# Kernel optimization log

Hardware: AMD Instinct MI355X
Metric: run time of the kernel (lower is better)

## Reference

```python
import jax, jax.numpy as jnp
import numpy as np

D_MODEL = 1024
N_HEADS = 16
HEAD_DIM = D_MODEL // N_HEADS


def setup_inputs() -> dict:
    key = jax.random.key(0)
    ks = jax.random.split(key, 5)
    B, S = 4, 2048
    scale = 1.0 / np.sqrt(D_MODEL)
    return {
        "x": jax.random.normal(ks[0], (B, S, D_MODEL), dtype=jnp.float32),
        "wq": jax.random.normal(ks[1], (D_MODEL, D_MODEL), dtype=jnp.float32) * scale,
        "wk": jax.random.normal(ks[2], (D_MODEL, D_MODEL), dtype=jnp.float32) * scale,
        "wv": jax.random.normal(ks[3], (D_MODEL, D_MODEL), dtype=jnp.float32) * scale,
        "wo": jax.random.normal(ks[4], (D_MODEL, D_MODEL), dtype=jnp.float32) * scale,
    }


def reference(x, wq, wk, wv, wo):
    B, S, _ = x.shape
    # projections: x @ W.T, then split heads -> [B, H, S, hd]
    def split_heads(t):
        return t.reshape(B, S, N_HEADS, HEAD_DIM).transpose(0, 2, 1, 3)

    q = split_heads(x @ wq.T)
    k = split_heads(x @ wk.T)
    v = split_heads(x @ wv.T)

    # scores [B, H, S, S], causal mask, stable softmax
    score = jnp.einsum("bhqd,bhkd->bhqk", q, k) / np.sqrt(HEAD_DIM)
    causal = jnp.tril(jnp.ones((S, S), dtype=bool))
    score = jnp.where(causal, score, -jnp.inf)
    attn = jax.nn.softmax(score, axis=-1)

    out = jnp.einsum("bhqk,bhkd->bhqd", attn, v)
    out = out.transpose(0, 2, 1, 3).reshape(B, S, D_MODEL)
    return out @ wo.T
```

## Files before the change

### kernel.cpp

```cpp
#include <hip/hip_runtime.h>
#include <type_traits>


typedef unsigned short u16;
typedef __attribute__((ext_vector_type(8))) short s8;
typedef __attribute__((ext_vector_type(4))) float f4;

#if __has_builtin(__builtin_amdgcn_exp2f)
#define EXP2(x) __builtin_amdgcn_exp2f(x)
#else
#define EXP2(x) exp2f(x)
#endif

__device__ __forceinline__ u16 f2bf(float f) {
    union { float f; unsigned u; } v; v.f = f;
    unsigned r = v.u + 0x7fffu + ((v.u >> 16) & 1u);
    return (u16)(r >> 16);
}

__device__ __forceinline__ unsigned pack_bf2(float a, float b) {
    return __builtin_amdgcn_perm(__float_as_uint(b), __float_as_uint(a),
                                 0x07060302u);
}

__device__ __forceinline__ void cp16(const void* g, void* l) {
    __builtin_amdgcn_global_load_lds(
        (const __attribute__((address_space(1))) unsigned int*)g,
        (__attribute__((address_space(3))) unsigned int*)l, 16, 0, 0);
}

__device__ __forceinline__ s8 load8f(const float* p) {
    const float4 lo = *(const float4*)p;
    const float4 hi = *(const float4*)(p + 4);
    s8 r;
    r[0] = (short)f2bf(lo.x); r[1] = (short)f2bf(lo.y);
    r[2] = (short)f2bf(lo.z); r[3] = (short)f2bf(lo.w);
    r[4] = (short)f2bf(hi.x); r[5] = (short)f2bf(hi.y);
    r[6] = (short)f2bf(hi.z); r[7] = (short)f2bf(hi.w);
    return r;
}

__global__ __launch_bounds__(256)
void f32_to_bf16(const float* __restrict__ in, u16* __restrict__ out, int n8)
{
    const int i = blockIdx.x * 256 + threadIdx.x;
    if (i < n8) *(s8*)(out + (size_t)i * 8) = load8f(in + (size_t)i * 8);
}

__global__ __launch_bounds__(256)
void cvt_w3(const float* __restrict__ a, const float* __restrict__ b2,
            const float* __restrict__ c3, u16* __restrict__ o, int per)
{
    const int y = blockIdx.y;
    const float* src = (y == 0) ? a : ((y == 1) ? b2 : c3);
    u16* dst = o + (size_t)y * per;
    const int i = blockIdx.x * 256 + threadIdx.x;
    *(s8*)(dst + (size_t)i * 8) = load8f(src + (size_t)i * 8);
}

template<typename TC>
__global__ __launch_bounds__(256)
void gemm_bb(const u16* __restrict__ A,
             const u16* __restrict__ W0, const u16* __restrict__ W1,
             const u16* __restrict__ W2,
             TC* __restrict__ C0, TC* __restrict__ C1,
             u16* __restrict__ VT, int K, float cscale)
{
    __shared__ u16 As[3][128 * 32];
    __shared__ u16 Bs[3][128 * 32];

    const int t  = threadIdx.x;
    const int bm = blockIdx.x;
    const int nglob = blockIdx.y * 128;

    const u16* W; int nloc, mode;
    if (nglob < 1024)      { W = W0; nloc = nglob;        mode = 0; }
    else if (nglob < 2048) { W = W1; nloc = nglob - 1024; mode = 1; }
    else                   { W = W2; nloc = nglob - 2048; mode = 2; }

    const int lane = t & 63, w = t >> 6;
    const int wm = (w >> 1) * 64, wn = (w & 1) * 64;
    const int quad = lane >> 4, l16 = lane & 15;

    const int sc = (((lane & 3) ^ ((lane >> 3) & 3))) * 8;
    const int sr = w * 32 + (lane >> 2);
    const u16* Ag0 = A + (size_t)(bm * 128 + sr) * K + sc;
    const u16* Ag1 = Ag0 + (size_t)16 * K;
    const u16* Wg0 = W + (size_t)(nloc + sr) * K + sc;
    const u16* Wg1 = Wg0 + (size_t)16 * K;
    const int la0 = (w * 32) * 32;
    const int la1 = (w * 32 + 16) * 32;

    const int ca = (quad ^ ((l16 >> 1) & 3)) * 8;

    auto stage = [&](int buf, int k0) {
        cp16(Ag0 + k0, &As[buf][la0]);
        cp16(Ag1 + k0, &As[buf][la1]);
        cp16(Wg0 + k0, &Bs[buf][la0]);
        cp16(Wg1 + k0, &Bs[buf][la1]);
    };

    f4 acc[4][4];
    for (int i = 0; i < 4; i++)
        for (int j = 0; j < 4; j++)
            acc[i][j] = (f4){0.f, 0.f, 0.f, 0.f};

    stage(0, 0);
    stage(1, 32);
    int cur = 0;
    for (int k0 = 0; k0 < K; k0 += 32) {
        if (k0 + 32 < K) asm volatile("s_waitcnt vmcnt(4)" ::: "memory");
        else             asm volatile("s_waitcnt vmcnt(0)" ::: "memory");
        __builtin_amdgcn_s_barrier();
        if (k0 + 96 <= K) stage((cur + 2) % 3, k0 + 64);

        s8 af[4], bf[4];
        for (int i = 0; i < 4; i++)
            af[i] = *(const s8*)&As[cur][(wm + i * 16 + l16) * 32 + ca];
        for (int j = 0; j < 4; j++)
            bf[j] = *(const s8*)&Bs[cur][(wn + j * 16 + l16) * 32 + ca];
        for (int i = 0; i < 4; i++)
            for (int j = 0; j < 4; j++)
                acc[i][j] = __builtin_amdgcn_mfma_f32_16x16x32_bf16(
                                af[i], bf[j], acc[i][j], 0, 0, 0);
        cur = (cur == 2) ? 0 : cur + 1;
    }

    if (mode == 2) {
        for (int i = 0; i < 4; i++) {
            const int row0 = bm * 128 + wm + i * 16 + quad * 4;
            const int b = row0 >> 11, s = row0 & 2047;
            for (int j = 0; j < 4; j++) {
                const int n = nloc + wn + j * 16 + l16;
                const int h = n >> 6, d = n & 63;
                unsigned lo = ((unsigned)f2bf(acc[i][j][1]) << 16) | f2bf(acc[i][j][0]);
                unsigned hi = ((unsigned)f2bf(acc[i][j][3]) << 16) | f2bf(acc[i][j][2]);
                *(uint2*)(VT + ((size_t)((b * 16 + h) * 64 + d)) * 2048 + s) =
                    make_uint2(lo, hi);
            }
        }
    } else {
        TC* C = (mode == 0) ? C0 : C1;
        const float cs = (mode == 0) ? cscale : 1.0f;
        for (int i = 0; i < 4; i++) {
            const int row = bm * 128 + wm + i * 16 + quad * 4;
            for (int j = 0; j < 4; j++) {
                const int col = nloc + wn + j * 16 + l16;
                for (int r = 0; r < 4; r++) {
                    const float val = acc[i][j][r] * cs;
                    if constexpr (std::is_same<TC, float>::value)
                        C[(size_t)(row + r) * 1024 + col] = val;
                    else
                        C[(size_t)(row + r) * 1024 + col] = f2bf(val);
                }
            }
        }
    }
}

#define PSTR 72

__global__ __launch_bounds__(256)
void attn_q32(const u16* __restrict__ Q, const u16* __restrict__ K,
              const u16* __restrict__ Vt, u16* __restrict__ O)
{
    __shared__ u16 Ks[2][64 * 64];
    __shared__ u16 Vs[2][64 * 64];
    __shared__ u16 Ps[4][32 * PSTR];

    const int bh = blockIdx.x;
    const int p  = 15 - blockIdx.y;
    const int h  = bh & 15, b = bh >> 4;

    const int t = threadIdx.x, lane = t & 63, w = t >> 6;
    const int quad = lane >> 4, l16 = lane & 15;
    const int colH = h * 64;

    const int q32 = 4 * p + w;
    const int ktw = q32 / 2 + 1;
    const int ktb = 2 * p + 2;

    s8 ones;
    for (int e = 0; e < 8; e++) ones[e] = (short)0x3F80;

    const int vrow = lane >> 3;
    const int scc  = ((lane & 7) ^ vrow) * 8;
    const int r0   = w * 16 + vrow;
    const u16* Kg0 = K  + ((size_t)b * 2048 + r0) * 1024 + colH + scc;
    const u16* Kg1 = Kg0 + (size_t)8 * 1024;
    const u16* Vg0 = Vt + ((size_t)(b * 16 + h) * 64 + r0) * 2048 + scc;
    const u16* Vg1 = Vg0 + (size_t)8 * 2048;
    const int kl0 = (w * 16) * 64;
    const int kl1 = (w * 16 + 8) * 64;

    auto stageKV = [&](int buf, int kt) {
        cp16(Kg0 + (size_t)kt * 65536, &Ks[buf][kl0]);
        cp16(Kg1 + (size_t)kt * 65536, &Ks[buf][kl1]);
        cp16(Vg0 + kt * 64, &Vs[buf][kl0]);
        cp16(Vg1 + kt * 64, &Vs[buf][kl1]);
    };

    const size_t rowQ0 = (size_t)b * 2048 + q32 * 32;

    s8 qf[2][2];
    for (int i = 0; i < 2; i++)
        for (int kk = 0; kk < 2; kk++)
            qf[i][kk] = *(const s8*)&Q[(rowQ0 + i * 16 + l16) * 1024 +
                                       colH + kk * 32 + quad * 8];

    f4 o_acc[2][4];
    f4 l_acc[2];
    for (int i = 0; i < 2; i++) {
        l_acc[i] = (f4){0.f, 0.f, 0.f, 0.f};
        for (int j = 0; j < 4; j++)
            o_acc[i][j] = (f4){0.f, 0.f, 0.f, 0.f};
    }

    stageKV(0, 0);
    int cur = 0;

    for (int kt = 0; kt < ktb; ++kt) {
        __syncthreads();
        if (kt + 1 < ktb) stageKV(cur ^ 1, kt + 1);

        if (kt < ktw) {
            f4 sa[4][2];
            for (int j = 0; j < 4; j++)
                for (int i = 0; i < 2; i++)
                    sa[j][i] = (f4){0.f, 0.f, 0.f, 0.f};
            for (int kk = 0; kk < 2; kk++) {
                s8 kf[4];
                for (int j = 0; j < 4; j++)
                    kf[j] = *(const s8*)&Ks[cur][(j * 16 + l16) * 64 +
                                            (((kk * 4 + quad) ^ (l16 & 7)) * 8)];
                for (int j = 0; j < 4; j++)
                    for (int i = 0; i < 2; i++)
                        sa[j][i] = __builtin_amdgcn_mfma_f32_16x16x32_bf16(
                                       kf[j], qf[i][kk], sa[j][i], 0, 0, 0);
            }

            const bool diag = (kt == ktw - 1);
            for (int i = 0; i < 2; i++) {
                const int q_l = i * 16 + l16;
                const int q_g = q32 * 32 + q_l;
                for (int j = 0; j < 4; j++) {
                    const int kv0 = kt * 64 + j * 16 + quad * 4;
                    float p0 = EXP2(sa[j][i][0]);
                    float p1 = EXP2(sa[j][i][1]);
                    float p2 = EXP2(sa[j][i][2]);
                    float p3 = EXP2(sa[j][i][3]);
                    if (diag) {
                        if (kv0 + 0 > q_g) p0 = 0.f;
                        if (kv0 + 1 > q_g) p1 = 0.f;
                        if (kv0 + 2 > q_g) p2 = 0.f;
                        if (kv0 + 3 > q_g) p3 = 0.f;
                    }
                    *(uint2*)&Ps[w][q_l * PSTR + j * 16 + quad * 4] =
                        make_uint2(pack_bf2(p0, p1), pack_bf2(p2, p3));
                }
            }

            for (int kk = 0; kk < 2; kk++) {
                s8 pf[2], vf[4];
                for (int i = 0; i < 2; i++)
                    pf[i] = *(const s8*)&Ps[w][(i * 16 + l16) * PSTR +
                                               kk * 32 + quad * 8];
                for (int jd = 0; jd < 4; jd++)
                    vf[jd] = *(const s8*)&Vs[cur][(jd * 16 + l16) * 64 +
                                            (((kk * 4 + quad) ^ (l16 & 7)) * 8)];
                for (int i = 0; i < 2; i++)
                    l_acc[i] = __builtin_amdgcn_mfma_f32_16x16x32_bf16(
                                   pf[i], ones, l_acc[i], 0, 0, 0);
                for (int i = 0; i < 2; i++)
                    for (int jd = 0; jd < 4; jd++)
                        o_acc[i][jd] = __builtin_amdgcn_mfma_f32_16x16x32_bf16(
                                           pf[i], vf[jd], o_acc[i][jd], 0, 0, 0);
            }
        }
        cur ^= 1;
    }

    for (int i = 0; i < 2; i++) {
        float rinv[4];
        for (int r = 0; r < 4; r++) rinv[r] = 1.0f / l_acc[i][r];
        for (int jd = 0; jd < 4; jd++)
            for (int r = 0; r < 4; r++) {
                const size_t row = rowQ0 + i * 16 + quad * 4 + r;
                O[row * 1024 + colH + jd * 16 + l16] =
                    f2bf(o_acc[i][jd][r] * rinv[r]);
            }
    }
}

extern "C" void kernel_launch(void* const* d_in, const int* in_sizes, int n_in,
                              void* d_out, int out_size, void* d_ws, size_t ws_size,
                              hipStream_t stream)
{
    const float* x  = (const float*)d_in[0];
    const float* wq = (const float*)d_in[1];
    const float* wk = (const float*)d_in[2];
    const float* wv = (const float*)d_in[3];
    const float* wo = (const float*)d_in[4];
    float* out = (float*)d_out;

    const size_t MD = (size_t)8192 * 1024;
    const size_t WD = (size_t)1024 * 1024;
    u16* Qb  = (u16*)d_ws;
    u16* Kb  = Qb + MD;
    u16* Vtb = Kb + MD;
    u16* Xb  = Vtb + MD;
    u16* Wqkv = (u16*)d_out;
    u16* Ob  = Qb;
    u16* Wob = Kb;

    f32_to_bf16<<<4096, 256, 0, stream>>>(x, Xb, (int)(MD / 8));

    cvt_w3<<<dim3(512, 3), 256, 0, stream>>>(wq, wk, wv, Wqkv, (int)WD);

    gemm_bb<u16><<<dim3(64, 24), 256, 0, stream>>>(
        Xb, Wqkv, Wqkv + WD, Wqkv + 2 * WD, Qb, Kb, Vtb, 1024, 0.18033688f);

    attn_q32<<<dim3(64, 16), 256, 0, stream>>>(Qb, Kb, Vtb, Ob);

    f32_to_bf16<<<512, 256, 0, stream>>>(wo, Wob, (int)(WD / 8));

    gemm_bb<float><<<dim3(64, 8), 256, 0, stream>>>(
        Ob, Wob, Wob, Wob, out, out, nullptr, 1024, 1.0f);
}
```

Before: 246.2 us.

## Widen attention blocks to 8 waves and merge input conversion launches

The attention kernel now runs 512 threads (8 waves) per block, each block covering 256 query rows, so every K/V tile staged in shared memory is reused by twice as many waves. The grid is halved and reordered to pair long and short causal rows. The x and weight fp32-to-bf16 conversions are also merged into one launch to cut launch overhead. In exchange, per-block shared memory grows and blocks are fewer and larger, and the causal imbalance within a block is wider.

```diff
diff --git a/kernel.cpp b/kernel.cpp
--- a/kernel.cpp
+++ b/kernel.cpp
@@ -48,14 +48,22 @@
 }
 
 __global__ __launch_bounds__(256)
-void cvt_w3(const float* __restrict__ a, const float* __restrict__ b2,
-            const float* __restrict__ c3, u16* __restrict__ o, int per)
-{
-    const int y = blockIdx.y;
-    const float* src = (y == 0) ? a : ((y == 1) ? b2 : c3);
-    u16* dst = o + (size_t)y * per;
+void cvt_xw(const float* __restrict__ x,
+            const float* __restrict__ wq, const float* __restrict__ wk,
+            const float* __restrict__ wv,
+            u16* __restrict__ Xb, u16* __restrict__ Wqkv)
+{
     const int i = blockIdx.x * 256 + threadIdx.x;
-    *(s8*)(dst + (size_t)i * 8) = load8f(src + (size_t)i * 8);
+    if (i < 1048576) {
+        *(s8*)(Xb + (size_t)i * 8) = load8f(x + (size_t)i * 8);
+    } else {
+        const int j = i - 1048576;
+        const int sel = j >> 17;
+        const int wi  = j & 131071;
+        const float* src = (sel == 0) ? wq : ((sel == 1) ? wk : wv);
+        *(s8*)(Wqkv + (size_t)sel * 1048576 + (size_t)wi * 8) =
+            load8f(src + (size_t)wi * 8);
+    }
 }
 
 template<typename TC>
@@ -160,44 +168,40 @@
 
 #define PSTR 72
 
-__global__ __launch_bounds__(256)
-void attn_q32(const u16* __restrict__ Q, const u16* __restrict__ K,
-              const u16* __restrict__ Vt, u16* __restrict__ O)
+__global__ __launch_bounds__(512)
+void attn8(const u16* __restrict__ Q, const u16* __restrict__ K,
+           const u16* __restrict__ Vt, u16* __restrict__ O)
 {
     __shared__ u16 Ks[2][64 * 64];
     __shared__ u16 Vs[2][64 * 64];
-    __shared__ u16 Ps[4][32 * PSTR];
+    __shared__ u16 Ps[8][32 * PSTR];
 
     const int bh = blockIdx.x;
-    const int p  = 15 - blockIdx.y;
+    const int yy = blockIdx.y;
+    const int p  = (yy < 4) ? (7 - yy) : (yy - 4);
     const int h  = bh & 15, b = bh >> 4;
 
     const int t = threadIdx.x, lane = t & 63, w = t >> 6;
     const int quad = lane >> 4, l16 = lane & 15;
     const int colH = h * 64;
 
-    const int q32 = 4 * p + w;
+    const int q32 = 8 * p + w;
     const int ktw = q32 / 2 + 1;
-    const int ktb = 2 * p + 2;
+    const int ktb = 4 * p + 4;
 
     s8 ones;
     for (int e = 0; e < 8; e++) ones[e] = (short)0x3F80;
 
     const int vrow = lane >> 3;
     const int scc  = ((lane & 7) ^ vrow) * 8;
-    const int r0   = w * 16 + vrow;
-    const u16* Kg0 = K  + ((size_t)b * 2048 + r0) * 1024 + colH + scc;
-    const u16* Kg1 = Kg0 + (size_t)8 * 1024;
-    const u16* Vg0 = Vt + ((size_t)(b * 16 + h) * 64 + r0) * 2048 + scc;
-    const u16* Vg1 = Vg0 + (size_t)8 * 2048;
-    const int kl0 = (w * 16) * 64;
-    const int kl1 = (w * 16 + 8) * 64;
+    const int r0   = w * 8 + vrow;
+    const u16* Kg = K  + ((size_t)b * 2048 + r0) * 1024 + colH + scc;
+    const u16* Vg = Vt + ((size_t)(b * 16 + h) * 64 + r0) * 2048 + scc;
+    const int klds = (w * 8) * 64;
 
     auto stageKV = [&](int buf, int kt) {
-        cp16(Kg0 + (size_t)kt * 65536, &Ks[buf][kl0]);
-        cp16(Kg1 + (size_t)kt * 65536, &Ks[buf][kl1]);
-        cp16(Vg0 + kt * 64, &Vs[buf][kl0]);
-        cp16(Vg1 + kt * 64, &Vs[buf][kl1]);
+        cp16(Kg + (size_t)kt * 65536, &Ks[buf][klds]);
+        cp16(Vg + kt * 64, &Vs[buf][klds]);
     };
 
     const size_t rowQ0 = (size_t)b * 2048 + q32 * 32;
@@ -313,14 +317,12 @@
     u16* Ob  = Qb;
     u16* Wob = Kb;
 
-    f32_to_bf16<<<4096, 256, 0, stream>>>(x, Xb, (int)(MD / 8));
-
-    cvt_w3<<<dim3(512, 3), 256, 0, stream>>>(wq, wk, wv, Wqkv, (int)WD);
+    cvt_xw<<<5632, 256, 0, stream>>>(x, wq, wk, wv, Xb, Wqkv);
 
     gemm_bb<u16><<<dim3(64, 24), 256, 0, stream>>>(
         Xb, Wqkv, Wqkv + WD, Wqkv + 2 * WD, Qb, Kb, Vtb, 1024, 0.18033688f);
 
-    attn_q32<<<dim3(64, 16), 256, 0, stream>>>(Qb, Kb, Vtb, Ob);
+    attn8<<<dim3(64, 8), 512, 0, stream>>>(Qb, Kb, Vtb, Ob);
 
     f32_to_bf16<<<512, 256, 0, stream>>>(wo, Wob, (int)(WD / 8));
 
```

Result: no change. 242.6 us (-1.5%).
